# Optimization experiments

Hardware: AMD Instinct MI355X
Metric: run time of the kernel (lower is better)

The kernel has to match this reference:

```python
import jax, jax.numpy as jnp
import numpy as np

B, DIM, NH, NB = 4, 1024, 4, 2
HD = DIM // NH


def _pe_enc(coords, gauss):
    # SAM PositionEmbeddingRandom._pe_encoding: coords in [0,1], shape (...,2)
    c = 2.0 * coords - 1.0
    c = c @ gauss                      # (..., DIM//2)
    c = (2.0 * np.pi) * c
    return jnp.concatenate([jnp.sin(c), jnp.cos(c)], axis=-1)  # (..., DIM)


def _ln(x, w, b):
    m = jnp.mean(x, axis=-1, keepdims=True)
    v = jnp.mean((x - m) ** 2, axis=-1, keepdims=True)
    return (x - m) * jax.lax.rsqrt(v + 1e-5) * w + b


def _attn(x, qkv_w, qkv_b, pw, pb):
    Bb, N, C = x.shape
    qkv = (x @ qkv_w + qkv_b).reshape(Bb, N, 3, NH, HD)
    q, k, v = qkv[:, :, 0], qkv[:, :, 1], qkv[:, :, 2]        # (B,N,H,D)
    a = jnp.einsum('bnhd,bmhd->bhnm', q * (HD ** -0.5), k)
    a = jax.nn.softmax(a, axis=-1)
    o = jnp.einsum('bhnm,bmhd->bnhd', a, v).reshape(Bb, N, C)
    return o @ pw + pb


def _block(i, first, x, x_pe, ctx, ctx_pe, p):
    # pe='normal', use_sep=True, init_values=0 -> LayerScale is identity
    if first:
        x = x + x_pe
        ctx = ctx + ctx_pe
    xl, cl = x.shape[1], ctx.shape[1]
    x = jnp.concatenate([x, p['sep'][i], ctx], axis=1)
    x = x + _attn(_ln(x, p['ln1_w'][i], p['ln1_b'][i]),
                  p['qkv_w'][i], p['qkv_b'][i], p['proj_w'][i], p['proj_b'][i])
    h = _ln(x, p['ln2_w'][i], p['ln2_b'][i])
    x = x + (jax.nn.gelu(h @ p['mlp_w1'][i] + p['mlp_b1'][i], approximate=False)
             @ p['mlp_w2'][i] + p['mlp_b2'][i])
    return x[:, :xl], x[:, xl + 1:xl + 1 + cl]


def _forward(image_embeddings, prompt_depth, gauss, d2f_w1, d2f_b1, d2f_w2, d2f_b2,
             p, idx_list, patch_h, patch_w):
    Hm, Wm = prompt_depth.shape[2], prompt_depth.shape[3]
    ys = (jnp.arange(patch_h, dtype=jnp.float32) + 0.5) / patch_h
    xs = (jnp.arange(patch_w, dtype=jnp.float32) + 0.5) / patch_w
    xx, yy = jnp.meshgrid(xs, ys)                              # (ph, pw)
    query_pe = _pe_enc(jnp.stack([xx, yy], axis=-1), gauss).reshape(1, -1, DIM)
    outs = []
    for b in range(image_embeddings.shape[0]):
        rows, cols = idx_list[b]
        if rows.size == 0:
            outs.append(image_embeddings[b:b + 1])
            continue
        # nonzero order: (row, col); module indexes pe with [col, row] = (x, y)
        pos = jnp.stack([(jnp.asarray(cols, dtype=jnp.float32) + 0.5) / Wm,
                         (jnp.asarray(rows, dtype=jnp.float32) + 0.5) / Hm], axis=-1)
        prompt_pe = _pe_enc(pos, gauss)[None]                  # (1, P, DIM)
        d = prompt_depth[b, 0][rows, cols][:, None]            # (P, 1)
        prompt = (jax.nn.gelu(d @ d2f_w1 + d2f_b1, approximate=False)
                  @ d2f_w2 + d2f_b2)[None]                     # (1, P, DIM)
        query = image_embeddings[b:b + 1]
        for i in range(NB):
            query, prompt = _block(i, i == 0, query, query_pe, prompt, prompt_pe, p)
        outs.append(query)
    return jnp.concatenate(outs, axis=0)


def setup_inputs() -> dict:
    key = jax.random.key(0)
    ks = jax.random.split(key, 12)
    f = jnp.float32
    rn = lambda k, s, sc=0.02: jax.random.normal(k, s, f) * sc
    return dict(
        image_embeddings=jax.random.normal(ks[0], (B, 1024, DIM), f),
        prompt_depth=jax.random.uniform(ks[1], (B, 1, 48, 48), dtype=f),
        prompt_mask=jax.random.randint(ks[2], (B, 1, 48, 48), 0, 2).astype(jnp.int32),
        patch_h=32, patch_w=32,
        gauss=jax.random.normal(ks[3], (2, DIM // 2), f),
        d2f_w1=rn(ks[4], (1, DIM // 2)), d2f_b1=jnp.zeros((DIM // 2,), f),
        d2f_w2=rn(ks[5], (DIM // 2, DIM)), d2f_b2=jnp.zeros((DIM,), f),
        sep=rn(ks[6], (NB, 1, 1, DIM), 1.0),
        ln1_w=jnp.ones((NB, DIM), f), ln1_b=jnp.zeros((NB, DIM), f),
        qkv_w=rn(ks[7], (NB, DIM, 3 * DIM)), qkv_b=jnp.zeros((NB, 3 * DIM), f),
        proj_w=rn(ks[8], (NB, DIM, DIM)), proj_b=jnp.zeros((NB, DIM), f),
        ln2_w=jnp.ones((NB, DIM), f), ln2_b=jnp.zeros((NB, DIM), f),
        mlp_w1=rn(ks[9], (NB, DIM, 4 * DIM)), mlp_b1=jnp.zeros((NB, 4 * DIM), f),
        mlp_w2=rn(ks[10], (NB, 4 * DIM, DIM)), mlp_b2=jnp.zeros((NB, DIM), f),
    )


def reference(image_embeddings, prompt_depth, prompt_mask, patch_h, patch_w,
              gauss, d2f_w1, d2f_b1, d2f_w2, d2f_b2, sep,
              ln1_w, ln1_b, qkv_w, qkv_b, proj_w, proj_b,
              ln2_w, ln2_b, mlp_w1, mlp_b1, mlp_w2, mlp_b2):
    m = np.asarray(prompt_mask)
    idx = [np.nonzero(m[b, 0] > 0) for b in range(m.shape[0])]
    p = dict(sep=sep, ln1_w=ln1_w, ln1_b=ln1_b, qkv_w=qkv_w, qkv_b=qkv_b,
             proj_w=proj_w, proj_b=proj_b, ln2_w=ln2_w, ln2_b=ln2_b,
             mlp_w1=mlp_w1, mlp_b1=mlp_b1, mlp_w2=mlp_w2, mlp_b2=mlp_b2)
    return _forward(image_embeddings, prompt_depth, gauss,
                    d2f_w1, d2f_b1, d2f_w2, d2f_b2, p, idx, int(patch_h), int(patch_w))
```

## Files before the change

kernel.cpp:

```cpp
#include <hip/hip_runtime.h>
#include <math.h>

#define NBATCH 4
#define DIM    1024
#define NHEAD  4
#define HD     256
#define NQ     1024
#define MASKN  2304
#define NMAX   3329
#define TWO_PI 6.283185307179586f

typedef unsigned short bf16_t;
typedef short bf16x8 __attribute__((ext_vector_type(8)));
typedef float f32x4  __attribute__((ext_vector_type(4)));

__device__ __forceinline__ float gelu_exact(float x) {
    return 0.5f * x * (1.0f + erff(x * 0.70710678118654752f));
}
__device__ __forceinline__ float bf2f(bf16_t h) {
    return __uint_as_float((unsigned)h << 16);
}
__device__ __forceinline__ bf16_t f2bf(float f) {
    unsigned u = __float_as_uint(f);
    return (bf16_t)((u + 0x7FFFu + ((u >> 16) & 1u)) >> 16);
}

__global__ __launch_bounds__(256)
void k_compact(const int* __restrict__ mask, int* __restrict__ cnt, int* __restrict__ pidx) {
    int b = blockIdx.x;
    __shared__ int sc;
    if (threadIdx.x == 0) sc = 0;
    __syncthreads();
    for (int c = threadIdx.x; c < MASKN; c += blockDim.x)
        if (mask[b * MASKN + c] > 0) {
            int p = atomicAdd(&sc, 1);
            pidx[b * MASKN + p] = c;
        }
    __syncthreads();
    if (threadIdx.x == 0) cnt[b] = sc;
}

__global__ __launch_bounds__(256)
void k_zerobias(float* __restrict__ z) {
    z[blockIdx.x * 256 + threadIdx.x] = 0.f;
}

__global__ __launch_bounds__(256)
void k_wt(const float* __restrict__ W, bf16_t* __restrict__ Wt, int K, int N) {
    __shared__ float T[64][65];
    int n0 = blockIdx.x * 64, k0 = blockIdx.y * 64;
    int tid = threadIdx.x;
    int lr = tid >> 4, lc = (tid & 15) * 4;
    #pragma unroll
    for (int i = 0; i < 4; ++i) {
        float4 v = *(const float4*)&W[(size_t)(k0 + lr + i * 16) * N + n0 + lc];
        T[lr + i * 16][lc + 0] = v.x; T[lr + i * 16][lc + 1] = v.y;
        T[lr + i * 16][lc + 2] = v.z; T[lr + i * 16][lc + 3] = v.w;
    }
    __syncthreads();
    int on = tid >> 2, ok = (tid & 3) * 16;
    bf16_t tmp[16];
    #pragma unroll
    for (int j = 0; j < 16; ++j) tmp[j] = f2bf(T[ok + j][on]);
    bf16_t* op = Wt + (size_t)(n0 + on) * K + k0 + ok;
    *(bf16x8*)op       = *(bf16x8*)&tmp[0];
    *(bf16x8*)(op + 8) = *(bf16x8*)&tmp[8];
}

__global__ __launch_bounds__(256)
void k_init_query(const float* __restrict__ emb, const float* __restrict__ gauss,
                  float* __restrict__ X) {
    int b = blockIdx.y, n = blockIdx.x, t = threadIdx.x;
    float fx = 2.0f * (((n & 31) + 0.5f) / 32.0f) - 1.0f;
    float fy = 2.0f * (((n >> 5) + 0.5f) / 32.0f) - 1.0f;
    const float* e = emb + ((size_t)b * NQ + n) * DIM;
    float* x = X + ((size_t)b * NMAX + n) * DIM;
    for (int d = t; d < 512; d += 256) {
        float ang = TWO_PI * (fx * gauss[d] + fy * gauss[512 + d]);
        float sn, cs; sincosf(ang, &sn, &cs);
        x[d]       = e[d] + sn;
        x[d + 512] = e[d + 512] + cs;
    }
}

__global__ __launch_bounds__(256)
void k_prompt_h(const float* __restrict__ depth, const float* __restrict__ w1,
                const float* __restrict__ b1, const int* __restrict__ cnt,
                const int* __restrict__ pidx, bf16_t* __restrict__ Hp) {
    int b = blockIdx.y, s = blockIdx.x, t = threadIdx.x;
    bf16_t* hp = Hp + ((size_t)b * MASKN + s) * 512;
    if (s >= cnt[b]) { hp[t] = 0; hp[t + 256] = 0; return; }
    int cell = pidx[b * MASKN + s];
    float d = depth[b * MASKN + cell];
    for (int j = t; j < 512; j += 256)
        hp[j] = f2bf(gelu_exact(fmaf(d, w1[j], b1[j])));
}

__global__ __launch_bounds__(256)
void k_pe_prompt(const float* __restrict__ gauss, const int* __restrict__ cnt,
                 const int* __restrict__ pidx, float* __restrict__ X) {
    int b = blockIdx.y, s = blockIdx.x, t = threadIdx.x;
    if (s >= cnt[b]) return;
    int cell = pidx[b * MASKN + s];
    int r = cell / 48, c = cell % 48;
    float fx = 2.0f * ((c + 0.5f) / 48.0f) - 1.0f;
    float fy = 2.0f * ((r + 0.5f) / 48.0f) - 1.0f;
    float* x = X + ((size_t)b * NMAX + 1025 + s) * DIM;
    for (int d = t; d < 512; d += 256) {
        float ang = TWO_PI * (fx * gauss[d] + fy * gauss[512 + d]);
        float sn, cs; sincosf(ang, &sn, &cs);
        x[d]       += sn;
        x[d + 512] += cs;
    }
}

__global__ __launch_bounds__(256)
void k_sep(float* __restrict__ X, const float* __restrict__ sep) {
    int b = blockIdx.x, t = threadIdx.x;
    float* x = X + ((size_t)b * NMAX + 1024) * DIM;
    *(float4*)&x[t * 4] = *(const float4*)&sep[t * 4];
}

__global__ __launch_bounds__(256)
void k_ln(const float* __restrict__ X, bf16_t* __restrict__ Xn,
          const float* __restrict__ w, const float* __restrict__ bb,
          const int* __restrict__ cnt) {
    int b = blockIdx.y, n = blockIdx.x;
    int Nb = 1025 + cnt[b];
    if (n >= Nb) return;
    int t = threadIdx.x;
    const float* x = X + ((size_t)b * NMAX + n) * DIM;
    float4 v = *(const float4*)&x[t * 4];
    float s = v.x + v.y + v.z + v.w;
    float q = v.x * v.x + v.y * v.y + v.z * v.z + v.w * v.w;
    #pragma unroll
    for (int off = 32; off > 0; off >>= 1) {
        s += __shfl_xor(s, off);
        q += __shfl_xor(q, off);
    }
    __shared__ float ss[4], sq[4];
    int wave = t >> 6, lane = t & 63;
    if (lane == 0) { ss[wave] = s; sq[wave] = q; }
    __syncthreads();
    s = ss[0] + ss[1] + ss[2] + ss[3];
    q = sq[0] + sq[1] + sq[2] + sq[3];
    float mean = s * (1.0f / DIM);
    float var  = q * (1.0f / DIM) - mean * mean;
    float rstd = 1.0f / sqrtf(var + 1e-5f);
    float4 ww = *(const float4*)&w[t * 4];
    float4 b4 = *(const float4*)&bb[t * 4];
    ushort4 o;
    o.x = f2bf((v.x - mean) * rstd * ww.x + b4.x);
    o.y = f2bf((v.y - mean) * rstd * ww.y + b4.y);
    o.z = f2bf((v.z - mean) * rstd * ww.z + b4.z);
    o.w = f2bf((v.w - mean) * rstd * ww.w + b4.w);
    *(ushort4*)&(Xn + ((size_t)b * NMAX + n) * DIM)[t * 4] = o;
}

template <int EPI, typename OutT>
__global__ __launch_bounds__(256)
void k_gemm_bt(const bf16_t* __restrict__ A, size_t bsA, int ldA,
               const bf16_t* __restrict__ Wt, int ldWt, const float* __restrict__ bias,
               OutT* __restrict__ Out, size_t bsO, int ldO,
               int K, const int* __restrict__ cnt, int bound_add, int rows_phys) {
    int b = blockIdx.z;
    int bound = cnt[b] + bound_add;
    int tr = blockIdx.y * 128;
    if (tr >= bound) return;
    int tc = blockIdx.x * 128;

    __shared__ bf16_t As[128][72];
    __shared__ bf16_t Bs[128][72];

    int tid  = threadIdx.x;
    int wave = tid >> 6, lane = tid & 63;
    int quad = lane >> 4, l16 = lane & 15;
    int wr = (wave >> 1) * 64, wc = (wave & 1) * 64;

    f32x4 acc[4][4];
    #pragma unroll
    for (int mi = 0; mi < 4; ++mi)
        #pragma unroll
        for (int ni = 0; ni < 4; ++ni)
            acc[mi][ni] = (f32x4){0.f, 0.f, 0.f, 0.f};

    const bf16_t* Ab = A + (size_t)b * bsA;
    int sr = tid >> 1;
    int sc = (tid & 1) * 32;

    for (int k0 = 0; k0 < K; k0 += 64) {
        __syncthreads();
        {
            int row = tr + sr;
            bf16x8 v[4];
            #pragma unroll
            for (int j = 0; j < 4; ++j) v[j] = (bf16x8){0,0,0,0,0,0,0,0};
            if (row < rows_phys) {
                const bf16_t* ap = Ab + (size_t)row * ldA + k0 + sc;
                #pragma unroll
                for (int j = 0; j < 4; ++j) v[j] = *(const bf16x8*)(ap + j * 8);
            }
            #pragma unroll
            for (int j = 0; j < 4; ++j) *(bf16x8*)&As[sr][sc + j * 8] = v[j];
        }
        {
            const bf16_t* bp = Wt + (size_t)(tc + sr) * ldWt + k0 + sc;
            #pragma unroll
            for (int j = 0; j < 4; ++j)
                *(bf16x8*)&Bs[sr][sc + j * 8] = *(const bf16x8*)(bp + j * 8);
        }
        __syncthreads();

        #pragma unroll
        for (int half = 0; half < 2; ++half) {
            int ko = half * 32 + quad * 8;
            bf16x8 af[4], bfr[4];
            #pragma unroll
            for (int mi = 0; mi < 4; ++mi)
                af[mi] = *(const bf16x8*)&As[wr + mi * 16 + l16][ko];
            #pragma unroll
            for (int ni = 0; ni < 4; ++ni)
                bfr[ni] = *(const bf16x8*)&Bs[wc + ni * 16 + l16][ko];
            #pragma unroll
            for (int mi = 0; mi < 4; ++mi)
                #pragma unroll
                for (int ni = 0; ni < 4; ++ni)
                    acc[mi][ni] = __builtin_amdgcn_mfma_f32_16x16x32_bf16(
                        af[mi], bfr[ni], acc[mi][ni], 0, 0, 0);
        }
    }

    OutT* Ob = Out + (size_t)b * bsO;
    #pragma unroll
    for (int ni = 0; ni < 4; ++ni) {
        int col = tc + wc + ni * 16 + l16;
        float bs = bias[col];
        #pragma unroll
        for (int mi = 0; mi < 4; ++mi) {
            int row0 = tr + wr + mi * 16 + quad * 4;
            #pragma unroll
            for (int r = 0; r < 4; ++r) {
                int row = row0 + r;
                if (row >= rows_phys) continue;
                float v = acc[mi][ni][r] + bs;
                if (EPI == 1) v = gelu_exact(v);
                OutT* op = Ob + (size_t)row * ldO + col;
                if (EPI == 2) v += *(const float*)op;
                if (sizeof(OutT) == 2) *(bf16_t*)op = f2bf(v);
                else                   *(float*)op  = v;
            }
        }
    }
}

__global__ __launch_bounds__(256)
void k_attn_mfma(const bf16_t* __restrict__ QKV, bf16_t* __restrict__ O,
                 const int* __restrict__ cnt) {
    int b = blockIdx.z, h = blockIdx.y;
    int Nb = 1025 + cnt[b];
    int qbase = blockIdx.x * 64;
    if (qbase >= Nb) return;

    __shared__ bf16_t Kt[32][264];
    __shared__ bf16_t Vt[256][40];
    __shared__ bf16_t Pt[4][16][40];

    int tid  = threadIdx.x;
    int wave = tid >> 6, lane = tid & 63;
    int quad = lane >> 4, l16 = lane & 15;

    int qrow  = qbase + wave * 16 + l16;
    int qrowc = qrow < NMAX ? qrow : NMAX - 1;
    const bf16_t* Qp = QKV + (size_t)b * NMAX * 3072 + (size_t)qrowc * 3072 + h * HD;
    bf16x8 qf[8];
    #pragma unroll
    for (int c = 0; c < 8; ++c)
        qf[c] = *(const bf16x8*)(Qp + c * 32 + quad * 8);

    f32x4 Oacc[16];
    #pragma unroll
    for (int n = 0; n < 16; ++n) Oacc[n] = (f32x4){0.f, 0.f, 0.f, 0.f};
    float l[4] = {0.f, 0.f, 0.f, 0.f};

    const bf16_t* Kg = QKV + (size_t)b * NMAX * 3072 + 1024 + h * HD;
    const bf16_t* Vg = QKV + (size_t)b * NMAX * 3072 + 2048 + h * HD;

    int krow_s = tid >> 3;
    int kd_s   = (tid & 7) * 8;
    int vd_s   = (tid >> 3) * 8;
    int vr_s   = (tid & 7) * 4;

    for (int kt = 0; kt < Nb; kt += 32) {
        __syncthreads();
        #pragma unroll
        for (int i = 0; i < 4; ++i) {
            int gk = kt + krow_s;
            int d  = kd_s + i * 64;
            bf16x8 v = (bf16x8){0,0,0,0,0,0,0,0};
            if (gk < Nb) v = *(const bf16x8*)(Kg + (size_t)gk * 3072 + d);
            *(bf16x8*)&Kt[krow_s][d] = v;
        }
        {
            bf16x8 vv[4];
            #pragma unroll
            for (int r = 0; r < 4; ++r) {
                int gk = kt + vr_s + r;
                vv[r] = (bf16x8){0,0,0,0,0,0,0,0};
                if (gk < Nb) vv[r] = *(const bf16x8*)(Vg + (size_t)gk * 3072 + vd_s);
            }
            #pragma unroll
            for (int j = 0; j < 8; ++j) {
                ushort4 pk;
                pk.x = (unsigned short)vv[0][j];
                pk.y = (unsigned short)vv[1][j];
                pk.z = (unsigned short)vv[2][j];
                pk.w = (unsigned short)vv[3][j];
                *(ushort4*)&Vt[vd_s + j][vr_s] = pk;
            }
        }
        __syncthreads();

        f32x4 c0 = (f32x4){0.f,0.f,0.f,0.f}, c1 = (f32x4){0.f,0.f,0.f,0.f};
        #pragma unroll
        for (int c = 0; c < 8; ++c) {
            bf16x8 kb0 = *(const bf16x8*)&Kt[l16     ][c * 32 + quad * 8];
            bf16x8 kb1 = *(const bf16x8*)&Kt[l16 + 16][c * 32 + quad * 8];
            c0 = __builtin_amdgcn_mfma_f32_16x16x32_bf16(qf[c], kb0, c0, 0, 0, 0);
            c1 = __builtin_amdgcn_mfma_f32_16x16x32_bf16(qf[c], kb1, c1, 0, 0, 0);
        }
        float ls[4];
        #pragma unroll
        for (int r = 0; r < 4; ++r) {
            float p0 = (kt + l16      < Nb) ? __expf(c0[r] * 0.0625f) : 0.f;
            float p1 = (kt + 16 + l16 < Nb) ? __expf(c1[r] * 0.0625f) : 0.f;
            Pt[wave][quad * 4 + r][l16]      = f2bf(p0);
            Pt[wave][quad * 4 + r][l16 + 16] = f2bf(p1);
            ls[r] = p0 + p1;
        }
        #pragma unroll
        for (int off = 1; off < 16; off <<= 1)
            #pragma unroll
            for (int r = 0; r < 4; ++r)
                ls[r] += __shfl_xor(ls[r], off);
        #pragma unroll
        for (int r = 0; r < 4; ++r) l[r] += ls[r];

        bf16x8 pa = *(const bf16x8*)&Pt[wave][l16][quad * 8];
        #pragma unroll
        for (int n = 0; n < 16; ++n) {
            bf16x8 vb = *(const bf16x8*)&Vt[n * 16 + l16][quad * 8];
            Oacc[n] = __builtin_amdgcn_mfma_f32_16x16x32_bf16(pa, vb, Oacc[n], 0, 0, 0);
        }
    }

    float inv[4];
    #pragma unroll
    for (int r = 0; r < 4; ++r) inv[r] = 1.0f / l[r];
    bf16_t* Op = O + (size_t)b * NMAX * DIM + h * HD;
    #pragma unroll
    for (int r = 0; r < 4; ++r) {
        int row = qbase + wave * 16 + quad * 4 + r;
        if (row < Nb) {
            bf16_t* op = Op + (size_t)row * DIM;
            #pragma unroll
            for (int n = 0; n < 16; ++n)
                op[n * 16 + l16] = f2bf(Oacc[n][r] * inv[r]);
        }
    }
}

__global__ __launch_bounds__(256)
void k_out(const float* __restrict__ X, const float* __restrict__ emb,
           const int* __restrict__ cnt, float* __restrict__ out) {
    int b = blockIdx.y, n = blockIdx.x, t = threadIdx.x;
    const float* s = (cnt[b] > 0) ? X + ((size_t)b * NMAX + n) * DIM
                                  : emb + ((size_t)b * NQ + n) * DIM;
    *(float4*)&out[((size_t)b * NQ + n) * DIM + t * 4] = *(const float4*)&s[t * 4];
}

extern "C" void kernel_launch(void* const* d_in, const int* in_sizes, int n_in,
                              void* d_out, int out_size, void* d_ws, size_t ws_size,
                              hipStream_t stream) {
    const float* emb    = (const float*)d_in[0];
    const float* depth  = (const float*)d_in[1];
    const int*   mask   = (const int*)d_in[2];
    const float* gauss  = (const float*)d_in[5];
    const float* d2f_w1 = (const float*)d_in[6];
    const float* d2f_b1 = (const float*)d_in[7];
    const float* d2f_w2 = (const float*)d_in[8];
    const float* d2f_b2 = (const float*)d_in[9];
    const float* sep    = (const float*)d_in[10];
    const float* ln1_w  = (const float*)d_in[11];
    const float* ln1_b  = (const float*)d_in[12];
    const float* qkv_w  = (const float*)d_in[13];
    const float* qkv_b  = (const float*)d_in[14];
    const float* proj_w = (const float*)d_in[15];
    const float* proj_b = (const float*)d_in[16];
    const float* ln2_w  = (const float*)d_in[17];
    const float* ln2_b  = (const float*)d_in[18];
    const float* mlp_w1 = (const float*)d_in[19];
    const float* mlp_b1 = (const float*)d_in[20];
    const float* mlp_w2 = (const float*)d_in[21];
    const float* mlp_b2 = (const float*)d_in[22];
    float* out = (float*)d_out;

    char* wsb = (char*)d_ws;
    int*    cnt   = (int*)wsb;
    int*    pidx  = (int*)(wsb + 256);
    float*  zbias = (float*)(wsb + 37120);
    float*  X     = (float*)(wsb + 41216);
    bf16_t* Xn    = (bf16_t*)(wsb + 54583552);
    bf16_t* Qb    = (bf16_t*)(wsb + 81854720);
    bf16_t* Wt_qkv = (bf16_t*)(wsb + 163668224);
    bf16_t* Wt_proj= (bf16_t*)(wsb + 169959680);
    bf16_t* Wt_m1  = (bf16_t*)(wsb + 172056832);
    bf16_t* Wt_m2  = (bf16_t*)(wsb + 180445440);
    if (ws_size < (size_t)188834048) return;

    k_compact<<<NBATCH, 256, 0, stream>>>(mask, cnt, pidx);
    k_zerobias<<<4, 256, 0, stream>>>(zbias);
    k_init_query<<<dim3(NQ, NBATCH), 256, 0, stream>>>(emb, gauss, X);
    k_prompt_h<<<dim3(MASKN, NBATCH), 256, 0, stream>>>(depth, d2f_w1, d2f_b1, cnt, pidx, Qb);
    k_wt<<<dim3(16, 8), 256, 0, stream>>>(d2f_w2, Wt_qkv, 512, DIM);
    k_gemm_bt<0, float><<<dim3(8, 18, NBATCH), 256, 0, stream>>>(
        Qb, (size_t)MASKN * 512, 512, Wt_qkv, 512, d2f_b2,
        X + (size_t)1025 * DIM, (size_t)NMAX * DIM, DIM, 512, cnt, 0, MASKN);
    k_pe_prompt<<<dim3(MASKN, NBATCH), 256, 0, stream>>>(gauss, cnt, pidx, X);

    for (int i = 0; i < 2; ++i) {
        k_wt<<<dim3(48, 16), 256, 0, stream>>>(qkv_w  + (size_t)i * DIM * 3072, Wt_qkv,  DIM, 3072);
        k_wt<<<dim3(16, 16), 256, 0, stream>>>(proj_w + (size_t)i * DIM * DIM,  Wt_proj, DIM, DIM);
        k_wt<<<dim3(64, 16), 256, 0, stream>>>(mlp_w1 + (size_t)i * DIM * 4096, Wt_m1,   DIM, 4096);
        k_wt<<<dim3(16, 64), 256, 0, stream>>>(mlp_w2 + (size_t)i * 4096 * DIM, Wt_m2,   4096, DIM);

        k_sep<<<NBATCH, 256, 0, stream>>>(X, sep + (size_t)i * DIM);
        k_ln<<<dim3(NMAX, NBATCH), 256, 0, stream>>>(X, Xn, ln1_w + i * DIM, ln1_b + i * DIM, cnt);
        k_gemm_bt<0, bf16_t><<<dim3(24, 27, NBATCH), 256, 0, stream>>>(
            Xn, (size_t)NMAX * DIM, DIM, Wt_qkv, DIM, qkv_b + (size_t)i * 3072,
            Qb, (size_t)NMAX * 3072, 3072, DIM, cnt, 1025, NMAX);
        k_attn_mfma<<<dim3(53, NHEAD, NBATCH), 256, 0, stream>>>(Qb, Xn, cnt);
        k_gemm_bt<2, float><<<dim3(8, 27, NBATCH), 256, 0, stream>>>(
            Xn, (size_t)NMAX * DIM, DIM, Wt_proj, DIM, proj_b + (size_t)i * DIM,
            X, (size_t)NMAX * DIM, DIM, DIM, cnt, 1025, NMAX);
        k_ln<<<dim3(NMAX, NBATCH), 256, 0, stream>>>(X, Xn, ln2_w + i * DIM, ln2_b + i * DIM, cnt);
        for (int c = 0; c < 2; ++c) {
            k_gemm_bt<1, bf16_t><<<dim3(16, 27, NBATCH), 256, 0, stream>>>(
                Xn, (size_t)NMAX * DIM, DIM,
                Wt_m1 + (size_t)c * 2048 * DIM, DIM,
                mlp_b1 + (size_t)i * 4096 + c * 2048,
                Qb, (size_t)NMAX * 2048, 2048, DIM, cnt, 1025, NMAX);
            k_gemm_bt<2, float><<<dim3(8, 27, NBATCH), 256, 0, stream>>>(
                Qb, (size_t)NMAX * 2048, 2048,
                Wt_m2 + (size_t)c * 2048, 4096,
                (c == 0) ? (mlp_b2 + (size_t)i * DIM) : zbias,
                X, (size_t)NMAX * DIM, DIM, 2048, cnt, 1025, NMAX);
        }
    }

    k_out<<<dim3(NQ, NBATCH), 256, 0, stream>>>(X, emb, cnt, out);
    (void)in_sizes; (void)n_in; (void)out_size;
}
```

Baseline: 1.720 ms.

## Double attention query tile to 128 rows and swizzle V-transpose LDS layout

The attention kernel now runs 512 threads (8 waves) per block, each block covering 128 query rows, so every K/V tile staged in LDS is reused by twice as many queries and global K/V traffic per query is halved. The K/V cooperative load is remapped to the larger thread count, and the transposed V tile gets an XOR swizzle on its column index to reduce LDS bank conflicts on both the transpose writes and the MFMA B-operand reads. The cost is half as many blocks in the grid (27x4x4), which lowers parallelism and occupancy, and larger blocks may leave CUs less evenly loaded.

```diff
diff --git a/kernel.cpp b/kernel.cpp
--- a/kernel.cpp
+++ b/kernel.cpp
@@ -253,17 +253,17 @@
     }
 }
 
-__global__ __launch_bounds__(256)
+__global__ __launch_bounds__(512)
 void k_attn_mfma(const bf16_t* __restrict__ QKV, bf16_t* __restrict__ O,
                  const int* __restrict__ cnt) {
     int b = blockIdx.z, h = blockIdx.y;
     int Nb = 1025 + cnt[b];
-    int qbase = blockIdx.x * 64;
+    int qbase = blockIdx.x * 128;
     if (qbase >= Nb) return;
 
     __shared__ bf16_t Kt[32][264];
     __shared__ bf16_t Vt[256][40];
-    __shared__ bf16_t Pt[4][16][40];
+    __shared__ bf16_t Pt[8][16][40];
 
     int tid  = threadIdx.x;
     int wave = tid >> 6, lane = tid & 63;
@@ -285,37 +285,39 @@
     const bf16_t* Kg = QKV + (size_t)b * NMAX * 3072 + 1024 + h * HD;
     const bf16_t* Vg = QKV + (size_t)b * NMAX * 3072 + 2048 + h * HD;
 
-    int krow_s = tid >> 3;
-    int kd_s   = (tid & 7) * 8;
-    int vd_s   = (tid >> 3) * 8;
-    int vr_s   = (tid & 7) * 4;
+    int krow_s = tid >> 4;
+    int kd_s   = (tid & 15) * 16;
+    int vdg    = tid >> 4;
+    int vkp    = (tid & 15) * 2;
+    int vsw    = (vdg & 3) * 8;
 
     for (int kt = 0; kt < Nb; kt += 32) {
         __syncthreads();
-        #pragma unroll
-        for (int i = 0; i < 4; ++i) {
+        {
             int gk = kt + krow_s;
-            int d  = kd_s + i * 64;
-            bf16x8 v = (bf16x8){0,0,0,0,0,0,0,0};
-            if (gk < Nb) v = *(const bf16x8*)(Kg + (size_t)gk * 3072 + d);
-            *(bf16x8*)&Kt[krow_s][d] = v;
+            bf16x8 v0 = (bf16x8){0,0,0,0,0,0,0,0};
+            bf16x8 v1 = (bf16x8){0,0,0,0,0,0,0,0};
+            if (gk < Nb) {
+                const bf16_t* kp = Kg + (size_t)gk * 3072 + kd_s;
+                v0 = *(const bf16x8*)kp;
+                v1 = *(const bf16x8*)(kp + 8);
+            }
+            *(bf16x8*)&Kt[krow_s][kd_s]     = v0;
+            *(bf16x8*)&Kt[krow_s][kd_s + 8] = v1;
         }
         {
-            bf16x8 vv[4];
-            #pragma unroll
-            for (int r = 0; r < 4; ++r) {
-                int gk = kt + vr_s + r;
-                vv[r] = (bf16x8){0,0,0,0,0,0,0,0};
-                if (gk < Nb) vv[r] = *(const bf16x8*)(Vg + (size_t)gk * 3072 + vd_s);
-            }
+            int g0 = kt + vkp, g1 = kt + vkp + 1;
+            bf16x8 r0 = (bf16x8){0,0,0,0,0,0,0,0};
+            bf16x8 r1 = (bf16x8){0,0,0,0,0,0,0,0};
+            if (g0 < Nb) r0 = *(const bf16x8*)(Vg + (size_t)g0 * 3072 + vdg * 8);
+            if (g1 < Nb) r1 = *(const bf16x8*)(Vg + (size_t)g1 * 3072 + vdg * 8);
+            int colw = vkp ^ vsw;
             #pragma unroll
             for (int j = 0; j < 8; ++j) {
-                ushort4 pk;
-                pk.x = (unsigned short)vv[0][j];
-                pk.y = (unsigned short)vv[1][j];
-                pk.z = (unsigned short)vv[2][j];
-                pk.w = (unsigned short)vv[3][j];
-                *(ushort4*)&Vt[vd_s + j][vr_s] = pk;
+                ushort2 pk;
+                pk.x = (unsigned short)r0[j];
+                pk.y = (unsigned short)r1[j];
+                *(ushort2*)&Vt[vdg * 8 + j][colw] = pk;
             }
         }
         __syncthreads();
@@ -348,7 +350,8 @@
         bf16x8 pa = *(const bf16x8*)&Pt[wave][l16][quad * 8];
         #pragma unroll
         for (int n = 0; n < 16; ++n) {
-            bf16x8 vb = *(const bf16x8*)&Vt[n * 16 + l16][quad * 8];
+            int sv = ((n * 2 + (l16 >> 3)) & 3) * 8;
+            bf16x8 vb = *(const bf16x8*)&Vt[n * 16 + l16][(quad * 8) ^ sv];
             Oacc[n] = __builtin_amdgcn_mfma_f32_16x16x32_bf16(pa, vb, Oacc[n], 0, 0, 0);
         }
     }
@@ -438,7 +441,7 @@
         k_gemm_bt<0, bf16_t><<<dim3(24, 27, NBATCH), 256, 0, stream>>>(
             Xn, (size_t)NMAX * DIM, DIM, Wt_qkv, DIM, qkv_b + (size_t)i * 3072,
             Qb, (size_t)NMAX * 3072, 3072, DIM, cnt, 1025, NMAX);
-        k_attn_mfma<<<dim3(53, NHEAD, NBATCH), 256, 0, stream>>>(Qb, Xn, cnt);
+        k_attn_mfma<<<dim3(27, NHEAD, NBATCH), 512, 0, stream>>>(Qb, Xn, cnt);
         k_gemm_bt<2, float><<<dim3(8, 27, NBATCH), 256, 0, stream>>>(
             Xn, (size_t)NMAX * DIM, DIM, Wt_proj, DIM, proj_b + (size_t)i * DIM,
             X, (size_t)NMAX * DIM, DIM, DIM, cnt, 1025, NMAX);
```

Result: slower. 1.954 ms (+13.6%).
